# Performance work log

Measured on AMD Instinct MI355X. Metric: run time of the kernel, lower is better.

The kernel has to match this reference:

```python
import jax, jax.numpy as jnp
import numpy as np

B, C, T = 128, 9, 2048
R = T // 4            # reduced_timesteps after two MaxPool1d(2)
N = B * R             # total graph nodes
E_SINGLE = 8192       # edges per sample graph (avg degree 16 over R nodes)
HID = 128
OUT = 12


def setup_inputs():
    key = jax.random.key(0)
    ks = jax.random.split(key, 14)
    x = jax.random.normal(ks[0], (B, C, T), jnp.float32)
    # per-sample graph, replicated with offset i*R per batch element (as in forward)
    single = jax.random.randint(ks[1], (2, E_SINGLE), 0, R)
    offsets = (jnp.arange(B) * R)[None, :, None]
    edge_index = (single[:, None, :] + offsets).reshape(2, -1)  # [2, B*E_SINGLE]

    def lin(k, fan_in, shape):
        return jax.random.normal(k, shape, jnp.float32) / np.sqrt(fan_in)

    return {
        "x": x,
        "edge_index": edge_index,
        "conv1_w": lin(ks[2], C * 5, (16, C, 5)),
        "conv1_b": jnp.zeros((16,), jnp.float32),
        "conv2_w": lin(ks[3], 16 * 5, (32, 16, 5)),
        "conv2_b": jnp.zeros((32,), jnp.float32),
        "gcn1_w": lin(ks[4], 32, (32, HID)),
        "gcn1_b": jnp.zeros((HID,), jnp.float32),
        "gcn2_w": lin(ks[5], HID, (HID, HID)),
        "gcn2_b": jnp.zeros((HID,), jnp.float32),
        "fc_w": lin(ks[6], HID, (HID, OUT)),
        "fc_b": jnp.zeros((OUT,), jnp.float32),
    }


def _gcn_conv(h, edge_index, w, b, n):
    # PyG GCNConv: linear -> add self-loops -> sym-normalized sum aggregation -> + bias
    h = h @ w
    loops = jnp.arange(n)
    row = jnp.concatenate([edge_index[0], loops])  # source
    col = jnp.concatenate([edge_index[1], loops])  # target (aggregation)
    deg = jax.ops.segment_sum(jnp.ones(col.shape, h.dtype), col, num_segments=n)
    dis = jnp.where(deg > 0, jax.lax.rsqrt(jnp.maximum(deg, 1e-12)), 0.0)
    norm = dis[row] * dis[col]                      # [E+N]
    out = jax.ops.segment_sum(norm[:, None] * h[row], col, num_segments=n)
    return out + b


def _temporal_conv(x, w1, b1, w2, b2):
    dn = ("NCH", "OIH", "NCH")
    h = jax.lax.conv_general_dilated(x, w1, (1,), [(2, 2)], dimension_numbers=dn)
    h = jax.nn.relu(h + b1[None, :, None])
    h = jax.lax.reduce_window(h, -jnp.inf, jax.lax.max, (1, 1, 2), (1, 1, 2), "VALID")
    h = jax.lax.conv_general_dilated(h, w2, (1,), [(2, 2)], dimension_numbers=dn)
    h = jax.nn.relu(h + b2[None, :, None])
    h = jax.lax.reduce_window(h, -jnp.inf, jax.lax.max, (1, 1, 2), (1, 1, 2), "VALID")
    return h  # [B, 32, R]


def reference(x, edge_index, conv1_w, conv1_b, conv2_w, conv2_b,
              gcn1_w, gcn1_b, gcn2_w, gcn2_b, fc_w, fc_b):
    h = _temporal_conv(x, conv1_w, conv1_b, conv2_w, conv2_b)   # [B, 32, R]
    nodes = h.transpose(0, 2, 1).reshape(B * R, 32)             # [N, 32]
    g = jax.nn.relu(_gcn_conv(nodes, edge_index, gcn1_w, gcn1_b, N))
    g = jax.nn.relu(_gcn_conv(g, edge_index, gcn2_w, gcn2_b, N))
    g = g.reshape(B, R, HID).mean(axis=1)                       # [B, HID]
    return g @ fc_w + fc_b                                      # [B, OUT]
```

## Files before the change

### kernel.cpp

```cpp
#include <hip/hip_runtime.h>
#include <hip/hip_bf16.h>

#define BB   128
#define CIN  9
#define TT   2048
#define RR   512
#define NN   (BB*RR)
#define HID  128
#define NOUT 12

typedef __attribute__((ext_vector_type(8))) short short8;
typedef __attribute__((ext_vector_type(4))) float f32x4;

static __device__ inline unsigned short f2bf(float f) {
    unsigned int u = __float_as_uint(f);
    unsigned int r = (u + 0x7fffu + ((u >> 16) & 1u)) >> 16;
    return (unsigned short)r;
}
static __device__ inline float bf2f(unsigned short u) {
    return __uint_as_float(((unsigned int)u) << 16);
}

__global__ __launch_bounds__(256) void k_convs(const float* __restrict__ x,
        const float* __restrict__ w1, const float* __restrict__ b1,
        const float* __restrict__ w2, const float* __restrict__ b2,
        float* __restrict__ nodes, float* __restrict__ meanbuf) {
    __shared__ float sx[CIN][524];
    __shared__ float s1[16][260];
    __shared__ float sw1[16 * CIN * 5];
    __shared__ float sb1[16];
    __shared__ float sw2[32 * 16 * 5];
    __shared__ float sb2[32];
    int b  = blockIdx.x >> 2;
    int r0 = (blockIdx.x & 3) * 128;
    int tid = threadIdx.x;

    if (blockIdx.x < 64) meanbuf[blockIdx.x * 256 + tid] = 0.f;

    for (int idx = tid; idx < CIN * 524; idx += 256) {
        int c = idx / 524, j = idx - c * 524;
        int g = 4 * r0 - 6 + j;
        float v = 0.f;
        if (g >= 0 && g < TT) v = x[(b * CIN + c) * TT + g];
        sx[c][j] = v;
    }
    for (int idx = tid; idx < 16 * CIN * 5; idx += 256) sw1[idx] = w1[idx];
    for (int idx = tid; idx < 32 * 16 * 5; idx += 256) sw2[idx] = w2[idx];
    if (tid < 16) sb1[tid] = b1[tid];
    if (tid < 32) sb2[tid] = b2[tid];
    __syncthreads();

    for (int idx = tid; idx < 16 * 260; idx += 256) {
        int c1 = idx / 260, pp = idx - c1 * 260;
        int p = 2 * r0 - 2 + pp;
        float val = 0.f;
        if (p >= 0 && p < 1024) {
            float a0 = sb1[c1], a1 = a0;
#pragma unroll
            for (int c = 0; c < CIN; ++c) {
                float xv[6];
#pragma unroll
                for (int k = 0; k < 6; ++k) xv[k] = sx[c][2 * pp + k];
#pragma unroll
                for (int k = 0; k < 5; ++k) {
                    float wv = sw1[(c1 * CIN + c) * 5 + k];
                    a0 += xv[k]     * wv;
                    a1 += xv[k + 1] * wv;
                }
            }
            val = fmaxf(fmaxf(a0, a1), 0.f);
        }
        s1[c1][pp] = val;
    }
    __syncthreads();

    int rl   = tid & 127;
    int half = tid >> 7;
    float acc0[16], acc1[16];
#pragma unroll
    for (int o = 0; o < 16; ++o) { float bv = sb2[half * 16 + o]; acc0[o] = bv; acc1[o] = bv; }
#pragma unroll
    for (int c = 0; c < 16; ++c) {
        float xv[6];
#pragma unroll
        for (int k = 0; k < 6; ++k) xv[k] = s1[c][2 * rl + k];
#pragma unroll
        for (int o = 0; o < 16; ++o) {
            int oo = half * 16 + o;
#pragma unroll
            for (int k = 0; k < 5; ++k) {
                float wv = sw2[(oo * 16 + c) * 5 + k];
                acc0[o] += xv[k]     * wv;
                acc1[o] += xv[k + 1] * wv;
            }
        }
    }
    int n = b * RR + r0 + rl;
#pragma unroll
    for (int o = 0; o < 16; ++o) {
        int oo = half * 16 + o;
        nodes[n * 32 + oo] = fmaxf(fmaxf(acc0[o], acc1[o]), 0.f);
    }
}

__global__ __launch_bounds__(512) void k_graph(const int* __restrict__ ei, int E,
        int es, int* __restrict__ rptr, float* __restrict__ dis,
        int* __restrict__ adj) {
    __shared__ int lcnt[512];
    __shared__ int sp[512];
    __shared__ int lcur[512];
    int t = threadIdx.x;
    lcnt[t] = 0;
    __syncthreads();
    for (int i = t; i < es; i += 512) atomicAdd(&lcnt[ei[E + i]], 1);
    __syncthreads();
    int c = lcnt[t];
    sp[t] = c;
    __syncthreads();
    for (int off = 1; off < 512; off <<= 1) {
        int v = sp[t];
        int add = (t >= off) ? sp[t - off] : 0;
        __syncthreads();
        sp[t] = v + add;
        __syncthreads();
    }
    int excl = sp[t] - c;
    rptr[t] = excl;
    if (t == 511) rptr[512] = es;
    dis[t] = rsqrtf((float)c + 1.0f);
    lcur[t] = excl;
    __syncthreads();
    for (int i = t; i < es; i += 512) {
        int row = ei[i], col = ei[E + i];
        int pos = atomicAdd(&lcur[col], 1);
        adj[pos] = row;
    }
}

__global__ __launch_bounds__(256) void k_gl1(const int* __restrict__ rptr,
        const int* __restrict__ adj, const float* __restrict__ dis,
        const float* __restrict__ nodes, const float* __restrict__ w,
        const float* __restrict__ bias, unsigned short* __restrict__ h16) {
    __shared__ float srow[32][32];
    __shared__ float sw[32 * 128];
    int bid = (blockIdx.x & 7) * 256 + (blockIdx.x >> 3);
    int tid = threadIdx.x;
    int nbase = bid * 32;
    int b = nbase >> 9;
    const float* hb = nodes + (size_t)b * RR * 32;

    {
        const float4* src = (const float4*)w;
        float4* dst = (float4*)sw;
#pragma unroll
        for (int i = 0; i < 4; ++i) dst[tid + i * 256] = src[tid + i * 256];
    }

    int ln   = tid >> 3;
    int lane = tid & 7;
    int r = (nbase & 511) + ln;
    int s = rptr[r], e = rptr[r + 1];
    float dn = dis[r];
    float4 acc = make_float4(0.f, 0.f, 0.f, 0.f);
    for (int base = s; base < e; base += 8) {
        int j = base + lane;
        int src = 0; float nd = 0.f;
        if (j < e) { src = adj[j]; nd = dis[src]; }
        int cnt = min(8, e - base);
        int k = 0;
        for (; k + 4 <= cnt; k += 4) {
            int   s0 = __shfl(src, k, 8),     s1 = __shfl(src, k + 1, 8);
            int   s2 = __shfl(src, k + 2, 8), s3 = __shfl(src, k + 3, 8);
            float n0 = __shfl(nd, k, 8),      n1 = __shfl(nd, k + 1, 8);
            float n2 = __shfl(nd, k + 2, 8),  n3 = __shfl(nd, k + 3, 8);
            float4 v0 = *(const float4*)&hb[(size_t)s0 * 32 + lane * 4];
            float4 v1 = *(const float4*)&hb[(size_t)s1 * 32 + lane * 4];
            float4 v2 = *(const float4*)&hb[(size_t)s2 * 32 + lane * 4];
            float4 v3 = *(const float4*)&hb[(size_t)s3 * 32 + lane * 4];
            float w0 = dn * n0, w1 = dn * n1, w2 = dn * n2, w3 = dn * n3;
            acc.x += w0*v0.x + w1*v1.x + w2*v2.x + w3*v3.x;
            acc.y += w0*v0.y + w1*v1.y + w2*v2.y + w3*v3.y;
            acc.z += w0*v0.z + w1*v1.z + w2*v2.z + w3*v3.z;
            acc.w += w0*v0.w + w1*v1.w + w2*v2.w + w3*v3.w;
        }
        for (; k < cnt; ++k) {
            int   sk = __shfl(src, k, 8);
            float nk = __shfl(nd, k, 8);
            float4 v = *(const float4*)&hb[(size_t)sk * 32 + lane * 4];
            float wgt = dn * nk;
            acc.x += wgt * v.x; acc.y += wgt * v.y;
            acc.z += wgt * v.z; acc.w += wgt * v.w;
        }
    }
    {
        float4 v = *(const float4*)&hb[(size_t)r * 32 + lane * 4];
        float wgt = dn * dn;
        acc.x += wgt * v.x; acc.y += wgt * v.y;
        acc.z += wgt * v.z; acc.w += wgt * v.w;
    }
    *(float4*)&srow[ln][lane * 4] = acc;
    __syncthreads();

    int fq = tid & 31;
    int ng = tid >> 5;
    float a[4][4];
#pragma unroll
    for (int j = 0; j < 4; ++j)
#pragma unroll
        for (int q = 0; q < 4; ++q) a[j][q] = 0.f;
#pragma unroll
    for (int c = 0; c < 32; ++c) {
        float4 wv = *(const float4*)&sw[c * 128 + fq * 4];
#pragma unroll
        for (int j = 0; j < 4; ++j) {
            float xc = srow[ng * 4 + j][c];
            a[j][0] += xc * wv.x; a[j][1] += xc * wv.y;
            a[j][2] += xc * wv.z; a[j][3] += xc * wv.w;
        }
    }
    float4 bv = *(const float4*)&bias[fq * 4];
#pragma unroll
    for (int j = 0; j < 4; ++j) {
        ushort4 o;
        o.x = f2bf(fmaxf(a[j][0] + bv.x, 0.f));
        o.y = f2bf(fmaxf(a[j][1] + bv.y, 0.f));
        o.z = f2bf(fmaxf(a[j][2] + bv.z, 0.f));
        o.w = f2bf(fmaxf(a[j][3] + bv.w, 0.f));
        *(ushort4*)&h16[(size_t)(nbase + ng * 4 + j) * 128 + fq * 4] = o;
    }
}

__global__ __launch_bounds__(256) void k_lin2(const unsigned short* __restrict__ g16,
        const float* __restrict__ w, unsigned short* __restrict__ h16) {
    __shared__ unsigned short srow[64][136];
    __shared__ unsigned short swT[128][136];
    int tid = threadIdx.x;
    int nbase = blockIdx.x * 64;

    {
        const ushort4* src = (const ushort4*)(g16 + (size_t)nbase * 128);
#pragma unroll
        for (int i = 0; i < 8; ++i) {
            int idx = tid + i * 256;
            int row = idx >> 5, col4 = idx & 31;
            ushort4 v = src[idx];
            *(ushort4*)&srow[row][col4 * 4] = v;
        }
    }
    {
        for (int i = 0; i < 64; ++i) {
            int idx = i * 256 + tid;
            int c = idx >> 7, f = idx & 127;
            swT[f][c] = f2bf(w[idx]);
        }
    }
    __syncthreads();

    int wv  = tid >> 6;
    int lane = tid & 63;
    int m0 = wv * 16;
    int l15 = lane & 15;
    int quad = lane >> 4;
    f32x4 acc[8];
#pragma unroll
    for (int nt = 0; nt < 8; ++nt) acc[nt] = (f32x4){0.f, 0.f, 0.f, 0.f};
#pragma unroll
    for (int kc = 0; kc < 4; ++kc) {
        int k0 = kc * 32 + quad * 8;
        short8 a = *(const short8*)&srow[m0 + l15][k0];
#pragma unroll
        for (int nt = 0; nt < 8; ++nt) {
            short8 b = *(const short8*)&swT[nt * 16 + l15][k0];
            acc[nt] = __builtin_amdgcn_mfma_f32_16x16x32_bf16(a, b, acc[nt], 0, 0, 0);
        }
    }
#pragma unroll
    for (int nt = 0; nt < 8; ++nt) {
#pragma unroll
        for (int r = 0; r < 4; ++r) {
            int row = m0 + quad * 4 + r;
            int col = nt * 16 + l15;
            h16[(size_t)(nbase + row) * 128 + col] = f2bf(acc[nt][r]);
        }
    }
}

__global__ __launch_bounds__(256) void k_gather128(const int* __restrict__ rptr,
        const int* __restrict__ adj, const float* __restrict__ dis,
        const unsigned short* __restrict__ h, const float* __restrict__ bias,
        float* __restrict__ meanbuf) {
    __shared__ float sred[8][128];
    int bid  = (blockIdx.x & 7) * 1024 + (blockIdx.x >> 3);
    int tid  = threadIdx.x;
    int g    = tid >> 5;
    int lane = tid & 31;
    int node = bid * 8 + g;
    int b = node >> 9;
    int r = node & 511;
    const unsigned short* hb = h + (size_t)b * RR * 128;
    int s = rptr[r], e = rptr[r + 1];
    float dn = dis[r];
    float4 acc = make_float4(0.f, 0.f, 0.f, 0.f);
    for (int base = s; base < e; base += 32) {
        int j = base + lane;
        int src = 0; float nd = 0.f;
        if (j < e) { src = adj[j]; nd = dis[src]; }
        int cnt = min(32, e - base);
        int k = 0;
        for (; k + 4 <= cnt; k += 4) {
            int   s0 = __shfl(src, k, 32),     s1 = __shfl(src, k + 1, 32);
            int   s2 = __shfl(src, k + 2, 32), s3 = __shfl(src, k + 3, 32);
            float n0 = __shfl(nd, k, 32),      n1 = __shfl(nd, k + 1, 32);
            float n2 = __shfl(nd, k + 2, 32),  n3 = __shfl(nd, k + 3, 32);
            ushort4 u0 = *(const ushort4*)&hb[(size_t)s0 * 128 + lane * 4];
            ushort4 u1 = *(const ushort4*)&hb[(size_t)s1 * 128 + lane * 4];
            ushort4 u2 = *(const ushort4*)&hb[(size_t)s2 * 128 + lane * 4];
            ushort4 u3 = *(const ushort4*)&hb[(size_t)s3 * 128 + lane * 4];
            float w0 = dn * n0, w1 = dn * n1, w2 = dn * n2, w3 = dn * n3;
            acc.x += w0*bf2f(u0.x) + w1*bf2f(u1.x) + w2*bf2f(u2.x) + w3*bf2f(u3.x);
            acc.y += w0*bf2f(u0.y) + w1*bf2f(u1.y) + w2*bf2f(u2.y) + w3*bf2f(u3.y);
            acc.z += w0*bf2f(u0.z) + w1*bf2f(u1.z) + w2*bf2f(u2.z) + w3*bf2f(u3.z);
            acc.w += w0*bf2f(u0.w) + w1*bf2f(u1.w) + w2*bf2f(u2.w) + w3*bf2f(u3.w);
        }
        for (; k < cnt; ++k) {
            int   sk = __shfl(src, k, 32);
            float nk = __shfl(nd, k, 32);
            ushort4 u = *(const ushort4*)&hb[(size_t)sk * 128 + lane * 4];
            float wgt = dn * nk;
            acc.x += wgt * bf2f(u.x); acc.y += wgt * bf2f(u.y);
            acc.z += wgt * bf2f(u.z); acc.w += wgt * bf2f(u.w);
        }
    }
    ushort4 u = *(const ushort4*)&hb[(size_t)r * 128 + lane * 4];
    float wgt = dn * dn;
    float4 bv = *(const float4*)&bias[lane * 4];
    acc.x = fmaxf(acc.x + wgt * bf2f(u.x) + bv.x, 0.f);
    acc.y = fmaxf(acc.y + wgt * bf2f(u.y) + bv.y, 0.f);
    acc.z = fmaxf(acc.z + wgt * bf2f(u.z) + bv.z, 0.f);
    acc.w = fmaxf(acc.w + wgt * bf2f(u.w) + bv.w, 0.f);
    *(float4*)&sred[g][lane * 4] = acc;
    __syncthreads();
    if (tid < 128) {
        float ssum = 0.f;
#pragma unroll
        for (int j = 0; j < 8; ++j) ssum += sred[j][tid];
        int sample = bid >> 6;
        unsafeAtomicAdd(&meanbuf[sample * 128 + tid], ssum * (1.0f / RR));
    }
}

__global__ __launch_bounds__(128) void k_fc(const float* __restrict__ meanbuf,
        const float* __restrict__ fw, const float* __restrict__ fb,
        float* __restrict__ out) {
    __shared__ float sm[HID];
    int b = blockIdx.x, f = threadIdx.x;
    sm[f] = meanbuf[b * HID + f];
    __syncthreads();
    if (f < NOUT) {
        float s = fb[f];
#pragma unroll
        for (int c = 0; c < HID; ++c) s += sm[c] * fw[c * NOUT + f];
        out[b * NOUT + f] = s;
    }
}

extern "C" void kernel_launch(void* const* d_in, const int* in_sizes, int n_in,
                              void* d_out, int out_size, void* d_ws, size_t ws_size,
                              hipStream_t stream) {
    const float* x   = (const float*)d_in[0];
    const int*   ei  = (const int*)d_in[1];
    const float* c1w = (const float*)d_in[2];
    const float* c1b = (const float*)d_in[3];
    const float* c2w = (const float*)d_in[4];
    const float* c2b = (const float*)d_in[5];
    const float* g1w = (const float*)d_in[6];
    const float* g1b = (const float*)d_in[7];
    const float* g2w = (const float*)d_in[8];
    const float* g2b = (const float*)d_in[9];
    const float* fw  = (const float*)d_in[10];
    const float* fb  = (const float*)d_in[11];
    float* out = (float*)d_out;
    int E  = in_sizes[1] / 2;
    int es = E / BB;

    char* ws = (char*)d_ws;
    float*          nodes   = (float*)(ws);
    unsigned short* bufA16  = (unsigned short*)(ws + (8u  << 20));
    unsigned short* bufC16  = (unsigned short*)(ws + (24u << 20));
    int*   rptr    = (int*)  (ws + (40u << 20));
    float* dis     = (float*)(ws + (40u << 20) + 4096);
    int*   adj     = (int*)  (ws + (40u << 20) + 8192);
    float* meanbuf = (float*)(ws + (41u << 20));

    k_convs<<<BB * 4, 256, 0, stream>>>(x, c1w, c1b, c2w, c2b, nodes, meanbuf);

    k_graph<<<1, 512, 0, stream>>>(ei, E, es, rptr, dis, adj);

    k_gl1<<<NN / 32, 256, 0, stream>>>(rptr, adj, dis, nodes, g1w, g1b, bufA16);

    k_lin2<<<NN / 64, 256, 0, stream>>>(bufA16, g2w, bufC16);
    k_gather128<<<NN / 8, 256, 0, stream>>>(rptr, adj, dis, bufC16, g2b, meanbuf);

    k_fc<<<BB, 128, 0, stream>>>(meanbuf, fw, fb, out);
}
```

Baseline: 200.7 us.

## Fuse graph build into conv kernel, retile convs, replace atomic mean with partials

The single-block graph-construction kernel is folded into the conv kernel as an extra block, so it runs alongside the convolutions instead of as its own serialized launch. The conv kernel is retiled to 1024 blocks of 512 threads, each covering 64 timesteps. Wave-uniform channel assignment lets the weights be read directly from global memory instead of being staged in shared memory, and each thread writes its four outputs as one float4. The atomic mean accumulation, together with the meanbuf zeroing it needed, is replaced by per-block partial sums that k_fc reduces. The trade-offs are a larger conv halo overhead and that the lone graph block may finish last.

```diff
diff --git a/kernel.cpp b/kernel.cpp
--- a/kernel.cpp
+++ b/kernel.cpp
@@ -21,120 +21,114 @@
     return __uint_as_float(((unsigned int)u) << 16);
 }
 
-__global__ __launch_bounds__(256) void k_convs(const float* __restrict__ x,
+__global__ __launch_bounds__(512) void k_convs(const float* __restrict__ x,
         const float* __restrict__ w1, const float* __restrict__ b1,
         const float* __restrict__ w2, const float* __restrict__ b2,
-        float* __restrict__ nodes, float* __restrict__ meanbuf) {
-    __shared__ float sx[CIN][524];
-    __shared__ float s1[16][260];
-    __shared__ float sw1[16 * CIN * 5];
-    __shared__ float sb1[16];
-    __shared__ float sw2[32 * 16 * 5];
-    __shared__ float sb2[32];
-    int b  = blockIdx.x >> 2;
-    int r0 = (blockIdx.x & 3) * 128;
+        float* __restrict__ nodes,
+        const int* __restrict__ ei, int E, int es,
+        int* __restrict__ rptr, float* __restrict__ dis, int* __restrict__ adj) {
+    __shared__ float sx[CIN][268];
+    __shared__ float s1[16][132];
+    __shared__ int lcnt[512];
+    __shared__ int sp[512];
+    __shared__ int lcur[512];
     int tid = threadIdx.x;
 
-    if (blockIdx.x < 64) meanbuf[blockIdx.x * 256 + tid] = 0.f;
-
-    for (int idx = tid; idx < CIN * 524; idx += 256) {
-        int c = idx / 524, j = idx - c * 524;
+    if (blockIdx.x == 1024) {
+        int t = tid;
+        lcnt[t] = 0;
+        __syncthreads();
+        for (int i = t; i < es; i += 512) atomicAdd(&lcnt[ei[E + i]], 1);
+        __syncthreads();
+        int c = lcnt[t];
+        sp[t] = c;
+        __syncthreads();
+        for (int off = 1; off < 512; off <<= 1) {
+            int v = sp[t];
+            int add = (t >= off) ? sp[t - off] : 0;
+            __syncthreads();
+            sp[t] = v + add;
+            __syncthreads();
+        }
+        int excl = sp[t] - c;
+        rptr[t] = excl;
+        if (t == 511) rptr[512] = es;
+        dis[t] = rsqrtf((float)c + 1.0f);
+        lcur[t] = excl;
+        __syncthreads();
+        for (int i = t; i < es; i += 512) {
+            int row = ei[i], col = ei[E + i];
+            int pos = atomicAdd(&lcur[col], 1);
+            adj[pos] = row;
+        }
+        return;
+    }
+
+    int b  = blockIdx.x >> 3;
+    int r0 = (blockIdx.x & 7) * 64;
+    int wv   = __builtin_amdgcn_readfirstlane(tid >> 6);
+    int lane = tid & 63;
+
+    for (int idx = tid; idx < CIN * 268; idx += 512) {
+        int c = idx / 268, j = idx - c * 268;
         int g = 4 * r0 - 6 + j;
         float v = 0.f;
         if (g >= 0 && g < TT) v = x[(b * CIN + c) * TT + g];
         sx[c][j] = v;
     }
-    for (int idx = tid; idx < 16 * CIN * 5; idx += 256) sw1[idx] = w1[idx];
-    for (int idx = tid; idx < 32 * 16 * 5; idx += 256) sw2[idx] = w2[idx];
-    if (tid < 16) sb1[tid] = b1[tid];
-    if (tid < 32) sb2[tid] = b2[tid];
-    __syncthreads();
-
-    for (int idx = tid; idx < 16 * 260; idx += 256) {
-        int c1 = idx / 260, pp = idx - c1 * 260;
-        int p = 2 * r0 - 2 + pp;
-        float val = 0.f;
-        if (p >= 0 && p < 1024) {
-            float a0 = sb1[c1], a1 = a0;
-#pragma unroll
-            for (int c = 0; c < CIN; ++c) {
-                float xv[6];
-#pragma unroll
-                for (int k = 0; k < 6; ++k) xv[k] = sx[c][2 * pp + k];
-#pragma unroll
-                for (int k = 0; k < 5; ++k) {
-                    float wv = sw1[(c1 * CIN + c) * 5 + k];
-                    a0 += xv[k]     * wv;
-                    a1 += xv[k + 1] * wv;
+    __syncthreads();
+
+#pragma unroll
+    for (int cc = 0; cc < 2; ++cc) {
+        int c1 = wv * 2 + cc;
+        float bias1 = b1[c1];
+        for (int pp = lane; pp < 132; pp += 64) {
+            int p = 2 * r0 - 2 + pp;
+            float val = 0.f;
+            if (p >= 0 && p < 1024) {
+                float a0 = bias1, a1 = bias1;
+#pragma unroll
+                for (int c = 0; c < CIN; ++c) {
+                    const float2* px = (const float2*)&sx[c][2 * pp];
+                    float2 q0 = px[0], q1 = px[1], q2 = px[2];
+                    const float* wp = &w1[(c1 * CIN + c) * 5];
+                    float k0 = wp[0], k1 = wp[1], k2 = wp[2], k3 = wp[3], k4 = wp[4];
+                    a0 += q0.x*k0 + q0.y*k1 + q1.x*k2 + q1.y*k3 + q2.x*k4;
+                    a1 += q0.y*k0 + q1.x*k1 + q1.y*k2 + q2.x*k3 + q2.y*k4;
                 }
+                val = fmaxf(fmaxf(a0, a1), 0.f);
             }
-            val = fmaxf(fmaxf(a0, a1), 0.f);
-        }
-        s1[c1][pp] = val;
-    }
-    __syncthreads();
-
-    int rl   = tid & 127;
-    int half = tid >> 7;
-    float acc0[16], acc1[16];
-#pragma unroll
-    for (int o = 0; o < 16; ++o) { float bv = sb2[half * 16 + o]; acc0[o] = bv; acc1[o] = bv; }
+            s1[c1][pp] = val;
+        }
+    }
+    __syncthreads();
+
+    int rl = lane;
+    float acc0[4], acc1[4];
+#pragma unroll
+    for (int o = 0; o < 4; ++o) {
+        float bv = b2[wv * 4 + o];
+        acc0[o] = bv; acc1[o] = bv;
+    }
 #pragma unroll
     for (int c = 0; c < 16; ++c) {
-        float xv[6];
-#pragma unroll
-        for (int k = 0; k < 6; ++k) xv[k] = s1[c][2 * rl + k];
-#pragma unroll
-        for (int o = 0; o < 16; ++o) {
-            int oo = half * 16 + o;
-#pragma unroll
-            for (int k = 0; k < 5; ++k) {
-                float wv = sw2[(oo * 16 + c) * 5 + k];
-                acc0[o] += xv[k]     * wv;
-                acc1[o] += xv[k + 1] * wv;
-            }
+        const float2* ps = (const float2*)&s1[c][2 * rl];
+        float2 q0 = ps[0], q1 = ps[1], q2 = ps[2];
+#pragma unroll
+        for (int o = 0; o < 4; ++o) {
+            const float* wp = &w2[((wv * 4 + o) * 16 + c) * 5];
+            float k0 = wp[0], k1 = wp[1], k2 = wp[2], k3 = wp[3], k4 = wp[4];
+            acc0[o] += q0.x*k0 + q0.y*k1 + q1.x*k2 + q1.y*k3 + q2.x*k4;
+            acc1[o] += q0.y*k0 + q1.x*k1 + q1.y*k2 + q2.x*k3 + q2.y*k4;
         }
     }
     int n = b * RR + r0 + rl;
-#pragma unroll
-    for (int o = 0; o < 16; ++o) {
-        int oo = half * 16 + o;
-        nodes[n * 32 + oo] = fmaxf(fmaxf(acc0[o], acc1[o]), 0.f);
-    }
-}
-
-__global__ __launch_bounds__(512) void k_graph(const int* __restrict__ ei, int E,
-        int es, int* __restrict__ rptr, float* __restrict__ dis,
-        int* __restrict__ adj) {
-    __shared__ int lcnt[512];
-    __shared__ int sp[512];
-    __shared__ int lcur[512];
-    int t = threadIdx.x;
-    lcnt[t] = 0;
-    __syncthreads();
-    for (int i = t; i < es; i += 512) atomicAdd(&lcnt[ei[E + i]], 1);
-    __syncthreads();
-    int c = lcnt[t];
-    sp[t] = c;
-    __syncthreads();
-    for (int off = 1; off < 512; off <<= 1) {
-        int v = sp[t];
-        int add = (t >= off) ? sp[t - off] : 0;
-        __syncthreads();
-        sp[t] = v + add;
-        __syncthreads();
-    }
-    int excl = sp[t] - c;
-    rptr[t] = excl;
-    if (t == 511) rptr[512] = es;
-    dis[t] = rsqrtf((float)c + 1.0f);
-    lcur[t] = excl;
-    __syncthreads();
-    for (int i = t; i < es; i += 512) {
-        int row = ei[i], col = ei[E + i];
-        int pos = atomicAdd(&lcur[col], 1);
-        adj[pos] = row;
-    }
+    float4 ov;
+    ov.x = fmaxf(fmaxf(acc0[0], acc1[0]), 0.f);
+    ov.y = fmaxf(fmaxf(acc0[1], acc1[1]), 0.f);
+    ov.z = fmaxf(fmaxf(acc0[2], acc1[2]), 0.f);
+    ov.w = fmaxf(fmaxf(acc0[3], acc1[3]), 0.f);
+    *(float4*)&nodes[n * 32 + wv * 4] = ov;
 }
 
 __global__ __launch_bounds__(256) void k_gl1(const int* __restrict__ rptr,
@@ -210,12 +204,12 @@
         for (int q = 0; q < 4; ++q) a[j][q] = 0.f;
 #pragma unroll
     for (int c = 0; c < 32; ++c) {
-        float4 wv = *(const float4*)&sw[c * 128 + fq * 4];
+        float4 wvv = *(const float4*)&sw[c * 128 + fq * 4];
 #pragma unroll
         for (int j = 0; j < 4; ++j) {
             float xc = srow[ng * 4 + j][c];
-            a[j][0] += xc * wv.x; a[j][1] += xc * wv.y;
-            a[j][2] += xc * wv.z; a[j][3] += xc * wv.w;
+            a[j][0] += xc * wvv.x; a[j][1] += xc * wvv.y;
+            a[j][2] += xc * wvv.z; a[j][3] += xc * wvv.w;
         }
     }
     float4 bv = *(const float4*)&bias[fq * 4];
@@ -288,7 +282,7 @@
 __global__ __launch_bounds__(256) void k_gather128(const int* __restrict__ rptr,
         const int* __restrict__ adj, const float* __restrict__ dis,
         const unsigned short* __restrict__ h, const float* __restrict__ bias,
-        float* __restrict__ meanbuf) {
+        float* __restrict__ partial) {
     __shared__ float sred[8][128];
     int bid  = (blockIdx.x & 7) * 1024 + (blockIdx.x >> 3);
     int tid  = threadIdx.x;
@@ -344,17 +338,19 @@
         float ssum = 0.f;
 #pragma unroll
         for (int j = 0; j < 8; ++j) ssum += sred[j][tid];
-        int sample = bid >> 6;
-        unsafeAtomicAdd(&meanbuf[sample * 128 + tid], ssum * (1.0f / RR));
-    }
-}
-
-__global__ __launch_bounds__(128) void k_fc(const float* __restrict__ meanbuf,
+        partial[(size_t)bid * 128 + tid] = ssum;
+    }
+}
+
+__global__ __launch_bounds__(128) void k_fc(const float* __restrict__ partial,
         const float* __restrict__ fw, const float* __restrict__ fb,
         float* __restrict__ out) {
     __shared__ float sm[HID];
     int b = blockIdx.x, f = threadIdx.x;
-    sm[f] = meanbuf[b * HID + f];
+    float acc = 0.f;
+#pragma unroll 8
+    for (int j = 0; j < 64; ++j) acc += partial[(size_t)(b * 64 + j) * 128 + f];
+    sm[f] = acc * (1.0f / RR);
     __syncthreads();
     if (f < NOUT) {
         float s = fb[f];
@@ -390,16 +386,15 @@
     int*   rptr    = (int*)  (ws + (40u << 20));
     float* dis     = (float*)(ws + (40u << 20) + 4096);
     int*   adj     = (int*)  (ws + (40u << 20) + 8192);
-    float* meanbuf = (float*)(ws + (41u << 20));
-
-    k_convs<<<BB * 4, 256, 0, stream>>>(x, c1w, c1b, c2w, c2b, nodes, meanbuf);
-
-    k_graph<<<1, 512, 0, stream>>>(ei, E, es, rptr, dis, adj);
+    float* partial = (float*)(ws + (41u << 20));
+
+    k_convs<<<BB * 8 + 1, 512, 0, stream>>>(x, c1w, c1b, c2w, c2b, nodes,
+                                            ei, E, es, rptr, dis, adj);
 
     k_gl1<<<NN / 32, 256, 0, stream>>>(rptr, adj, dis, nodes, g1w, g1b, bufA16);
 
     k_lin2<<<NN / 64, 256, 0, stream>>>(bufA16, g2w, bufC16);
-    k_gather128<<<NN / 8, 256, 0, stream>>>(rptr, adj, dis, bufC16, g2b, meanbuf);
-
-    k_fc<<<BB, 128, 0, stream>>>(meanbuf, fw, fb, out);
-}
+    k_gather128<<<NN / 8, 256, 0, stream>>>(rptr, adj, dis, bufC16, g2b, partial);
+
+    k_fc<<<BB, 128, 0, stream>>>(partial, fw, fb, out);
+}
```

After: 176.0 us. 1.14x faster.
